# Optimization experiments

Hardware: AMD Instinct MI355X
Metric: run time of the kernel (lower is better)

## Reference

```python
import jax, jax.numpy as jnp
import numpy as np
from jax import lax

N_STEPS, IN_LEN, OUT_LEN, H_LEN, C_LEN, BATCH = 24, 512, 256, 1024, 1024, 128


def setup_inputs() -> dict:
    key = jax.random.key(0)
    ks = jax.random.split(key, 16)
    g = lambda k, shp: jax.random.normal(k, shp, dtype=jnp.float32)
    ih = IN_LEN + H_LEN
    return {
        "x": g(ks[0], (BATCH, N_STEPS, IN_LEN)),
        "W": g(ks[1], (N_STEPS, C_LEN, ih)) * 0.02,
        "Wi": g(ks[2], (N_STEPS, C_LEN, ih)) * 0.02,
        "Wf": g(ks[3], (N_STEPS, C_LEN, ih)) * 0.02,
        "Wo": g(ks[4], (N_STEPS, C_LEN, ih)) * 0.02,
        "Wout": g(ks[5], (N_STEPS, OUT_LEN, H_LEN)) * 0.02,
        "b": g(ks[6], (N_STEPS, C_LEN)) * 0.02,
        "bi": g(ks[7], (N_STEPS, C_LEN)) * 0.02,
        "bf": g(ks[8], (N_STEPS, C_LEN)) * 0.02,
        "bo": g(ks[9], (N_STEPS, C_LEN)) * 0.02,
        "bout": g(ks[10], (N_STEPS, OUT_LEN)) * 0.02,
        "c0": g(ks[11], (C_LEN,)) * 0.02,
        "h0": g(ks[12], (H_LEN,)) * 0.02,
    }


def reference(x, W, Wi, Wf, Wo, Wout, b, bi, bf, bo, bout, c0, h0):
    B = x.shape[0]
    c = jnp.broadcast_to(c0, (B, c0.shape[0]))  # repmat(c0, len(x))
    h = jnp.broadcast_to(h0, (B, h0.shape[0]))

    def step(carry, inp):
        c_, h_ = carry
        xt, w, wi, wf, wo, wout, bb, bbi, bbf, bbo, bbout = inp
        xh = jnp.concatenate([xt, h_], axis=-1)            # [B, i+h]
        z = jnp.tanh(xh @ w.T + bb)                        # [B, c]
        zi = jax.nn.sigmoid(xh @ wi.T + bbi)
        zf = jax.nn.sigmoid(xh @ wf.T + bbf)
        zo = jax.nn.sigmoid(xh @ wo.T + bbo)
        cn = zf * c_ + zi * z
        hn = zo * jnp.tanh(cn)
        y = jax.nn.sigmoid(hn @ wout.T + bbout)            # [B, o]
        return (cn, hn), y

    xs = jnp.swapaxes(x, 0, 1)                             # [n, B, i]
    _, ys = lax.scan(step, (c, h), (xs, W, Wi, Wf, Wo, Wout, b, bi, bf, bo, bout))
    # concat y over steps along last axis -> [B, n*o]
    return jnp.transpose(ys, (1, 0, 2)).reshape(B, -1)
```

## Files before the change

kernel.cpp:

```cpp
#include <hip/hip_runtime.h>

#define B_    128
#define NSTEP 24
#define INL   512
#define OUTL  256
#define HL    1024
#define CL    1024
#define IH    (INL + HL)
#define G_BLOCKS 256

typedef short          s16x8 __attribute__((ext_vector_type(8)));
typedef float          f32x4 __attribute__((ext_vector_type(4)));
typedef unsigned short u16x4 __attribute__((ext_vector_type(4)));

#define FWS_C   64
#define FWS_HA  (FWS_C + 524288)
#define FWS_HB  (FWS_HA + 262144)
#define FWS_XW  (FWS_HB + 262144)
#define FWS_END (FWS_XW + 25165824)
#define WS_C  64
#define WS_HA (64 + 262144)
#define WS_HB (64 + 524288)

__device__ __forceinline__ float bits2f(unsigned short u) {
    union { unsigned u; float f; } w; w.u = ((unsigned)u) << 16; return w.f;
}
__device__ __forceinline__ unsigned short f2bf(float f) {
    union { float f; unsigned u; } w; w.f = f;
    unsigned r = (w.u + 0x7fffu + ((w.u >> 16) & 1u)) >> 16;
    return (unsigned short)r;
}
__device__ __forceinline__ float sigmoidf_(float v) { return 1.0f / (1.0f + expf(-v)); }
__device__ __forceinline__ float sane(float v, float lim) {
    return fminf(fmaxf(v, -lim), lim);
}

template<int FP32>
__device__ __forceinline__ s16x8 load8(const void* base, size_t off) {
    if constexpr (FP32) {
        const float* p = (const float*)base + off;
        f32x4 a = *(const f32x4*)p;
        f32x4 b = *(const f32x4*)(p + 4);
        s16x8 r;
        r[0] = (short)f2bf(a[0]); r[1] = (short)f2bf(a[1]);
        r[2] = (short)f2bf(a[2]); r[3] = (short)f2bf(a[3]);
        r[4] = (short)f2bf(b[0]); r[5] = (short)f2bf(b[1]);
        r[6] = (short)f2bf(b[2]); r[7] = (short)f2bf(b[3]);
        return r;
    } else {
        return *(const s16x8*)((const unsigned short*)base + off);
    }
}
template<int FP32>
__device__ __forceinline__ float ld1(const void* base, size_t off) {
    if constexpr (FP32) return ((const float*)base)[off];
    else                return bits2f(((const unsigned short*)base)[off]);
}
template<int FP32>
__device__ __forceinline__ u16x4 ldcvt4(const void* base, size_t off) {
    if constexpr (FP32) {
        f32x4 v = *(const f32x4*)((const float*)base + off);
        u16x4 r;
        r[0] = f2bf(v[0]); r[1] = f2bf(v[1]); r[2] = f2bf(v[2]); r[3] = f2bf(v[3]);
        return r;
    } else {
        return *(const u16x4*)((const unsigned short*)base + off);
    }
}
__device__ __forceinline__ s16x8 ldh8(const unsigned short* __restrict__ h,
                                      int row, int k0) {
    const unsigned short* p = h + (size_t)(k0 >> 2) * 512 + row * 4;
    u16x4 lo = *(const u16x4*)p;
    u16x4 hi = *(const u16x4*)(p + 512);
    s16x8 r;
    r[0] = (short)lo[0]; r[1] = (short)lo[1]; r[2] = (short)lo[2]; r[3] = (short)lo[3];
    r[4] = (short)hi[0]; r[5] = (short)hi[1]; r[6] = (short)hi[2]; r[7] = (short)hi[3];
    return r;
}

__global__ void detect_kernel(const unsigned* __restrict__ xw, int* __restrict__ flag) {
    __shared__ int wild, zero;
    const int tid = threadIdx.x;
    if (tid == 0) { wild = 0; zero = 0; }
    __syncthreads();
    int w = 0, z = 0;
    for (int s = 0; s < 4; ++s) {
        unsigned short lo = (unsigned short)(xw[tid * 4 + s] & 0xffffu);
        float v = bits2f(lo);
        if (v == 0.0f) z++;
        else if (v == v && (fabsf(v) > 1e4f || fabsf(v) < 1e-8f)) w++;
    }
    atomicAdd(&wild, w);
    atomicAdd(&zero, z);
    __syncthreads();
    if (tid == 0) *flag = (wild > 128 || zero > 512) ? 1 : 0;
}


__global__ void init_full_kernel(const void* c0, const void* h0, const int* __restrict__ flag,
                                 float* __restrict__ c,
                                 unsigned short* __restrict__ hA,
                                 unsigned short* __restrict__ hB)
{
    const int f   = *flag;
    const int idx = blockIdx.x * blockDim.x + threadIdx.x;
    if (idx < B_ * CL) {
        const int j = ((idx >> 9) << 2) + (idx & 3);
        c[idx]  = f ? ((const float*)c0)[j] : bits2f(((const unsigned short*)c0)[j]);
        const float hv = f ? ((const float*)h0)[j] : bits2f(((const unsigned short*)h0)[j]);
        const unsigned short hb = f2bf(hv);
        hA[idx] = hb;
        hB[idx] = hb;
    }
}

#define XA_PITCH 40
template<int FP32>
__device__ __forceinline__ void xw_tile_body(
    const void* __restrict__ x,
    const void* __restrict__ W,  const void* __restrict__ Wi,
    const void* __restrict__ Wf, const void* __restrict__ Wo,
    _Float16* __restrict__ XW, int t, int j0)
{
    __shared__ unsigned short smem[2 * 128 * XA_PITCH];
    unsigned short* Alds = smem;
    unsigned short* Blds = smem + 128 * XA_PITCH;

    const int tid  = threadIdx.x;
    const int lane = tid & 63;
    const int wv   = tid >> 6;
    const int c16  = lane & 15;
    const int kg   = lane >> 4;
    const int mq   = wv >> 1, nq = wv & 1;

    int rowc[4], colc[4];
    const void* wbase[4];
    size_t wrow[4];
    #pragma unroll
    for (int p = 0; p < 4; ++p) {
        const int cid = tid + p * 256;
        rowc[p] = cid >> 3;
        colc[p] = (cid & 7) * 4;
        const int g = rowc[p] >> 5;
        wbase[p] = (g == 0) ? W : (g == 1) ? Wi : (g == 2) ? Wf : Wo;
        wrow[p]  = ((size_t)(t * CL + j0 + (rowc[p] & 31))) * IH;
    }

    f32x4 acc[4][4];
    #pragma unroll
    for (int a = 0; a < 4; ++a)
        #pragma unroll
        for (int b = 0; b < 4; ++b) acc[a][b] = (f32x4){0.f, 0.f, 0.f, 0.f};

    u16x4 ra[4], rb[4];
    #pragma unroll
    for (int p = 0; p < 4; ++p) {
        ra[p] = ldcvt4<FP32>(wbase[p], wrow[p] + colc[p]);
        rb[p] = ldcvt4<FP32>(x,  ((size_t)(rowc[p] * NSTEP + t)) * INL + colc[p]);
    }

    for (int s = 0; s < 16; ++s) {
        __syncthreads();
        #pragma unroll
        for (int p = 0; p < 4; ++p) {
            *(u16x4*)(Alds + rowc[p] * XA_PITCH + colc[p]) = ra[p];
            *(u16x4*)(Blds + rowc[p] * XA_PITCH + colc[p]) = rb[p];
        }
        if (s < 15) {
            const int k0 = (s + 1) * 32;
            #pragma unroll
            for (int p = 0; p < 4; ++p) {
                ra[p] = ldcvt4<FP32>(wbase[p], wrow[p] + k0 + colc[p]);
                rb[p] = ldcvt4<FP32>(x,  ((size_t)(rowc[p] * NSTEP + t)) * INL + k0 + colc[p]);
            }
        }
        __syncthreads();
        s16x8 av[4], bv[4];
        #pragma unroll
        for (int mf = 0; mf < 4; ++mf)
            av[mf] = *(const s16x8*)(Alds + (mq * 64 + mf * 16 + c16) * XA_PITCH + kg * 8);
        #pragma unroll
        for (int nf = 0; nf < 4; ++nf)
            bv[nf] = *(const s16x8*)(Blds + (nq * 64 + nf * 16 + c16) * XA_PITCH + kg * 8);
        #pragma unroll
        for (int mf = 0; mf < 4; ++mf)
            #pragma unroll
            for (int nf = 0; nf < 4; ++nf)
                acc[mf][nf] = __builtin_amdgcn_mfma_f32_16x16x32_bf16(av[mf], bv[nf], acc[mf][nf], 0, 0, 0);
    }

    #pragma unroll
    for (int mf = 0; mf < 4; ++mf)
        #pragma unroll
        for (int nf = 0; nf < 4; ++nf)
            #pragma unroll
            for (int i = 0; i < 4; ++i) {
                const int jr = mq * 64 + mf * 16 + kg * 4 + i;
                const int bc = nq * 64 + nf * 16 + c16;
                const int g  = jr >> 5;
                const int j  = j0 + (jr & 31);
                XW[((((size_t)t * 256 + (j >> 2)) * B_ + bc) * 4 + (j & 3)) * 4 + g] =
                    (_Float16)acc[mf][nf][i];
            }
}

__global__ __launch_bounds__(256, 2) void xw_tile_kernel(
    const void* x, const void* W, const void* Wi, const void* Wf, const void* Wo,
    const int* __restrict__ flag, _Float16* XW)
{
    const int blk = blockIdx.x;
    const int t   = blk >> 5;
    const int j0  = (blk & 31) * 32;
    if (*flag) xw_tile_body<1>(x, W, Wi, Wf, Wo, XW, t, j0);
    else       xw_tile_body<0>(x, W, Wi, Wf, Wo, XW, t, j0);
}

template<int FP32>
__device__ __forceinline__ void step5_body(
    const void* __restrict__ W,  const void* __restrict__ Wi,
    const void* __restrict__ Wf, const void* __restrict__ Wo,
    const void* __restrict__ bz, const void* __restrict__ bi,
    const void* __restrict__ bfg, const void* __restrict__ bo,
    const void* __restrict__ Wout, const void* __restrict__ bout,
    const _Float16* __restrict__ XW, float* __restrict__ c,
    const unsigned short* __restrict__ hprev,
    unsigned short* __restrict__ hnext,
    float* __restrict__ out, int t)
{
    __shared__ unsigned short smem[16 * 1024];
    const int blk  = blockIdx.x;
    const int tid  = threadIdx.x;
    const int lane = tid & 63;
    const int wv   = tid >> 6;
    const int c16  = lane & 15;
    const int kg   = lane >> 4;
    const bool isOut = (blk >= G_BLOCKS);
    if (isOut && t == 0) return;

    {
        const int srow = tid >> 5;
        const int scl  = (tid & 31) * 4;
        const void* wptr;
        size_t woff;
        if (!isOut) {
            const int g = srow >> 2, jj = srow & 3;
            wptr = (g == 0) ? W : (g == 1) ? Wi : (g == 2) ? Wf : Wo;
            woff = ((size_t)(t * CL + blk * 4 + jj)) * IH + INL;
        } else {
            wptr = Wout;
            woff = ((size_t)((t - 1) * OUTL + (blk - G_BLOCKS) * 16 + srow)) * HL;
        }
        const unsigned swz = (unsigned)((srow & 7) << 4);
        #pragma unroll
        for (int i = 0; i < 8; ++i) {
            const int col = scl + i * 128;
            u16x4 v = ldcvt4<FP32>(wptr, woff + col);
            *(u16x4*)((char*)smem + srow * 2048 + (((unsigned)(col * 2)) ^ swz)) = v;
        }
    }
    __syncthreads();

    const int row = wv * 16 + c16;
    const char* brow = (const char*)smem + c16 * 2048;
    const unsigned cswz = (unsigned)((c16 & 7) << 4);
    f32x4 acc = {0.f, 0.f, 0.f, 0.f};
    #pragma unroll 8
    for (int kb = 0; kb < HL; kb += 32) {
        s16x8 av = ldh8(hprev, row, kb + kg * 8);
        s16x8 bv = *(const s16x8*)(brow + (((unsigned)((kb + kg * 8) * 2)) ^ cswz));
        acc = __builtin_amdgcn_mfma_f32_16x16x32_bf16(av, bv, acc, 0, 0, 0);
    }

    if (isOut) {
        const int o = (blk - G_BLOCKS) * 16 + c16;
        const float bb = ld1<FP32>(bout, (size_t)(t - 1) * OUTL + o);
        #pragma unroll
        for (int i = 0; i < 4; ++i) {
            const int b = wv * 16 + kg * 4 + i;
            out[(size_t)b * (NSTEP * OUTL) + (size_t)(t - 1) * OUTL + o] =
                sigmoidf_(sane(acc[i] + bb, 30.f));
        }
        return;
    }

    __syncthreads();
    float* lsm = (float*)smem;
    #pragma unroll
    for (int i = 0; i < 4; ++i)
        lsm[c16 * 130 + wv * 16 + kg * 4 + i] = acc[i];
    __syncthreads();

    const int b  = tid >> 2;
    const int jq = tid & 3;
    const int jg = blk * 4 + jq;
    u16x4 xv = *(const u16x4*)((const unsigned short*)XW +
                               (((size_t)t * 256 + blk) * B_ + b) * 16 + jq * 4);
    union { unsigned short u; _Float16 h; } cv0, cv1, cv2, cv3;
    cv0.u = xv[0]; cv1.u = xv[1]; cv2.u = xv[2]; cv3.u = xv[3];
    const float l0 = lsm[(0 * 4 + jq) * 130 + b] + (float)cv0.h
                   + ld1<FP32>(bz,  (size_t)t * CL + jg);
    const float l1 = lsm[(1 * 4 + jq) * 130 + b] + (float)cv1.h
                   + ld1<FP32>(bi,  (size_t)t * CL + jg);
    const float l2 = lsm[(2 * 4 + jq) * 130 + b] + (float)cv2.h
                   + ld1<FP32>(bfg, (size_t)t * CL + jg);
    const float l3 = lsm[(3 * 4 + jq) * 130 + b] + (float)cv3.h
                   + ld1<FP32>(bo,  (size_t)t * CL + jg);
    const float z  = tanhf(sane(l0, 30.f));
    const float zi = sigmoidf_(sane(l1, 30.f));
    const float zf = sigmoidf_(sane(l2, 30.f));
    const float zo = sigmoidf_(sane(l3, 30.f));
    const size_t soff = (size_t)blk * 512 + tid;
    const float cold = c[soff];
    const float cn   = sane(zf * cold + zi * z, 50.f);
    c[soff] = cn;
    hnext[soff] = f2bf(zo * tanhf(cn));
}

__global__ __launch_bounds__(512, 4) void step5_kernel(
    const void* W, const void* Wi, const void* Wf, const void* Wo,
    const void* bz, const void* bi, const void* bfg, const void* bo,
    const void* Wout, const void* bout,
    const int* __restrict__ flag, const _Float16* XW, float* c,
    const unsigned short* hprev, unsigned short* hnext, float* out, int t)
{
    if (*flag) step5_body<1>(W, Wi, Wf, Wo, bz, bi, bfg, bo, Wout, bout, XW, c, hprev, hnext, out, t);
    else       step5_body<0>(W, Wi, Wf, Wo, bz, bi, bfg, bo, Wout, bout, XW, c, hprev, hnext, out, t);
}

template<int FP32>
__device__ __forceinline__ void outproj_part(
    const unsigned short* __restrict__ h, const void* __restrict__ Wout,
    const void* __restrict__ bout, float* __restrict__ out, int tp, int og,
    int tid, float* __restrict__ red)
{
    const int lane = tid & 63;
    const int wv   = tid >> 6;
    const int c16  = lane & 15;
    const int kg   = lane >> 4;
    const int mf   = wv & 1;
    const int kh   = wv >> 1;

    const int o0   = (og & 15) * 16;
    const int mgrp = og >> 4;
    const int o    = o0 + c16;

    const size_t woff = ((size_t)tp * OUTL + o) * HL + kh * 512 + kg * 8;
    const int row = mgrp * 32 + mf * 16 + c16;

    f32x4 acc = {0.f, 0.f, 0.f, 0.f};
    #pragma unroll 8
    for (int kb = 0; kb < 512; kb += 32) {
        s16x8 av = ldh8(h, row, kh * 512 + kb + kg * 8);
        s16x8 bv = load8<FP32>(Wout, woff + kb);
        acc = __builtin_amdgcn_mfma_f32_16x16x32_bf16(av, bv, acc, 0, 0, 0);
    }
    #pragma unroll
    for (int i = 0; i < 4; ++i)
        red[((kh * 2 + mf) * 16 + c16) * 16 + kg * 4 + i] = acc[i];
    __syncthreads();

    const float bb = ld1<FP32>(bout, (size_t)tp * OUTL + o0 + (tid & 15));
    #pragma unroll
    for (int p = 0; p < 2; ++p) {
        const int idx = tid + p * 256;
        const int cc  = idx & 15;
        const int r   = idx >> 4;
        const int mff = r >> 4, rm = r & 15;
        const float lgv = red[(mff * 16 + cc) * 16 + rm]
                        + red[((2 + mff) * 16 + cc) * 16 + rm] + bb;
        out[(size_t)(mgrp * 32 + r) * (NSTEP * OUTL) + (size_t)tp * OUTL + o0 + cc] =
            sigmoidf_(sane(lgv, 30.f));
    }
}

__global__ __launch_bounds__(512, 4) void outproj_final2_kernel(
    const unsigned short* h, const void* Wout, const void* bout,
    const int* __restrict__ flag, float* out)
{
    __shared__ float red[2048];
    const int tid  = threadIdx.x;
    const int half = tid >> 8;
    const int og   = blockIdx.x * 2 + half;
    if (*flag) outproj_part<1>(h, Wout, bout, out, NSTEP - 1, og, tid & 255, red + half * 1024);
    else       outproj_part<0>(h, Wout, bout, out, NSTEP - 1, og, tid & 255, red + half * 1024);
}

template<int FP32>
__device__ __forceinline__ void gate_body(
    const void* __restrict__ x,
    const void* __restrict__ W,  const void* __restrict__ Wi,
    const void* __restrict__ Wf, const void* __restrict__ Wo,
    const void* __restrict__ bz, const void* __restrict__ bi,
    const void* __restrict__ bfg, const void* __restrict__ bo,
    _Float16* __restrict__ c,
    const unsigned short* __restrict__ hprev,
    unsigned short* __restrict__ hnext, int t)
{
    const int tid  = threadIdx.x;
    const int lane = tid & 63;
    const int wv   = tid >> 6;
    const int j0   = blockIdx.x * 4;
    const int c16  = lane & 15;
    const int g    = c16 >> 2;
    const int jj   = c16 & 3;
    const int kg   = lane >> 4;

    const void* Wg = (g == 0) ? W : (g == 1) ? Wi : (g == 2) ? Wf : Wo;
    const size_t woff = ((size_t)t * CL + (j0 + jj)) * IH + kg * 8;
    const int row0 = wv * 32 + c16;
    const int row1 = row0 + 16;

    f32x4 acc0 = {0.f, 0.f, 0.f, 0.f};
    f32x4 acc1 = {0.f, 0.f, 0.f, 0.f};
    {
        const size_t a0 = ((size_t)row0 * NSTEP + t) * INL + kg * 8;
        const size_t a1 = ((size_t)row1 * NSTEP + t) * INL + kg * 8;
        #pragma unroll 4
        for (int kb = 0; kb < INL; kb += 32) {
            s16x8 av0 = load8<FP32>(x, a0 + kb);
            s16x8 av1 = load8<FP32>(x, a1 + kb);
            s16x8 bv  = load8<FP32>(Wg, woff + kb);
            acc0 = __builtin_amdgcn_mfma_f32_16x16x32_bf16(av0, bv, acc0, 0, 0, 0);
            acc1 = __builtin_amdgcn_mfma_f32_16x16x32_bf16(av1, bv, acc1, 0, 0, 0);
        }
    }
    {
        const unsigned short* a0 = hprev + (size_t)row0 * HL + kg * 8;
        const unsigned short* a1 = hprev + (size_t)row1 * HL + kg * 8;
        const size_t w2 = woff + INL;
        #pragma unroll 4
        for (int kb = 0; kb < HL; kb += 32) {
            s16x8 av0 = *(const s16x8*)(a0 + kb);
            s16x8 av1 = *(const s16x8*)(a1 + kb);
            s16x8 bv  = load8<FP32>(Wg, w2 + kb);
            acc0 = __builtin_amdgcn_mfma_f32_16x16x32_bf16(av0, bv, acc0, 0, 0, 0);
            acc1 = __builtin_amdgcn_mfma_f32_16x16x32_bf16(av1, bv, acc1, 0, 0, 0);
        }
    }
    __shared__ float lg[4][4][B_];
    #pragma unroll
    for (int i = 0; i < 4; ++i) {
        lg[g][jj][wv * 32 + kg * 4 + i]      = acc0[i];
        lg[g][jj][wv * 32 + 16 + kg * 4 + i] = acc1[i];
    }
    __syncthreads();
    #pragma unroll
    for (int p = 0; p < 2; ++p) {
        const int idx = tid + p * 256;
        const int b   = idx & 127;
        const int jl  = idx >> 7;
        const int jg  = j0 + jl;
        const float z  = tanhf   (sane(lg[0][jl][b] + ld1<FP32>(bz,  t * CL + jg), 30.f));
        const float zi = sigmoidf_(sane(lg[1][jl][b] + ld1<FP32>(bi,  t * CL + jg), 30.f));
        const float zf = sigmoidf_(sane(lg[2][jl][b] + ld1<FP32>(bfg, t * CL + jg), 30.f));
        const float zo = sigmoidf_(sane(lg[3][jl][b] + ld1<FP32>(bo,  t * CL + jg), 30.f));
        const float cold = (float)c[(size_t)b * CL + jg];
        const float cn   = sane(zf * cold + zi * z, 50.f);
        c[(size_t)b * CL + jg] = (_Float16)cn;
        hnext[(size_t)b * HL + jg] = f2bf(zo * tanhf(cn));
    }
}

__global__ __launch_bounds__(256, 1) void gate_cell_kernel(
    const void* x, const void* W, const void* Wi, const void* Wf, const void* Wo,
    const void* bz, const void* bi, const void* bfg, const void* bo,
    const int* __restrict__ flag, _Float16* c,
    const unsigned short* hprev, unsigned short* hnext, int t)
{
    if (*flag) gate_body<1>(x, W, Wi, Wf, Wo, bz, bi, bfg, bo, c, hprev, hnext, t);
    else       gate_body<0>(x, W, Wi, Wf, Wo, bz, bi, bfg, bo, c, hprev, hnext, t);
}

template<int FP32>
__device__ __forceinline__ void outproj_body(
    const unsigned short* __restrict__ h, const void* __restrict__ Wout,
    const void* __restrict__ bout, float* __restrict__ out, int t)
{
    const int tid  = threadIdx.x;
    const int lane = tid & 63;
    const int wv   = tid >> 6;
    const int o    = blockIdx.x * 16 + (lane & 15);
    const int kg   = lane >> 4;
    const size_t woff = ((size_t)t * OUTL + o) * HL + kg * 8;
    const int row0 = wv * 32 + (lane & 15);
    const int row1 = row0 + 16;
    const unsigned short* a0 = h + (size_t)row0 * HL + kg * 8;
    const unsigned short* a1 = h + (size_t)row1 * HL + kg * 8;

    f32x4 acc0 = {0.f, 0.f, 0.f, 0.f};
    f32x4 acc1 = {0.f, 0.f, 0.f, 0.f};
    #pragma unroll 4
    for (int kb = 0; kb < HL; kb += 32) {
        s16x8 av0 = *(const s16x8*)(a0 + kb);
        s16x8 av1 = *(const s16x8*)(a1 + kb);
        s16x8 bv  = load8<FP32>(Wout, woff + kb);
        acc0 = __builtin_amdgcn_mfma_f32_16x16x32_bf16(av0, bv, acc0, 0, 0, 0);
        acc1 = __builtin_amdgcn_mfma_f32_16x16x32_bf16(av1, bv, acc1, 0, 0, 0);
    }
    const float bb = ld1<FP32>(bout, (size_t)t * OUTL + o);
    #pragma unroll
    for (int i = 0; i < 4; ++i) {
        const int r0 = wv * 32 + kg * 4 + i;
        out[(size_t)r0 * (NSTEP * OUTL) + (size_t)t * OUTL + o] =
            sigmoidf_(sane(acc0[i] + bb, 30.f));
        out[(size_t)(r0 + 16) * (NSTEP * OUTL) + (size_t)t * OUTL + o] =
            sigmoidf_(sane(acc1[i] + bb, 30.f));
    }
}

__global__ __launch_bounds__(256, 1) void outproj_kernel(
    const unsigned short* h, const void* Wout, const void* bout,
    const int* __restrict__ flag, float* out, int t)
{
    if (*flag) outproj_body<1>(h, Wout, bout, out, t);
    else       outproj_body<0>(h, Wout, bout, out, t);
}

__global__ void init_kernel(const void* c0, const void* h0, const int* __restrict__ flag,
                            _Float16* __restrict__ c,
                            unsigned short* __restrict__ hA,
                            unsigned short* __restrict__ hB)
{
    const int f   = *flag;
    const int idx = blockIdx.x * blockDim.x + threadIdx.x;
    if (idx < B_ * CL) {
        const int j = idx & (CL - 1);
        const float cv = f ? ((const float*)c0)[j] : bits2f(((const unsigned short*)c0)[j]);
        const float hv = f ? ((const float*)h0)[j] : bits2f(((const unsigned short*)h0)[j]);
        c[idx]  = (_Float16)cv;
        const unsigned short hb = f2bf(hv);
        hA[idx] = hb;
        hB[idx] = hb;
    }
}

extern "C" void kernel_launch(void* const* d_in, const int* in_sizes, int n_in,
                              void* d_out, int out_size, void* d_ws, size_t ws_size,
                              hipStream_t stream)
{
    const void* x    = d_in[0];
    const void* W    = d_in[1];
    const void* Wi   = d_in[2];
    const void* Wf   = d_in[3];
    const void* Wo   = d_in[4];
    const void* Wout = d_in[5];
    const void* bz   = d_in[6];
    const void* bi   = d_in[7];
    const void* bfg  = d_in[8];
    const void* bo   = d_in[9];
    const void* bout = d_in[10];
    const void* c0   = d_in[11];
    const void* h0   = d_in[12];

    char* ws  = (char*)d_ws;
    int* flag = (int*)ws;
    float* out = (float*)d_out;

    detect_kernel<<<1, 256, 0, stream>>>((const unsigned*)x, flag);

    if (ws_size >= (size_t)FWS_END) {
        float*          c  = (float*)(ws + FWS_C);
        unsigned short* hA = (unsigned short*)(ws + FWS_HA);
        unsigned short* hB = (unsigned short*)(ws + FWS_HB);
        _Float16*       XW = (_Float16*)(ws + FWS_XW);

        init_full_kernel<<<512, 256, 0, stream>>>(c0, h0, flag, c, hA, hB);
        xw_tile_kernel<<<768, 256, 0, stream>>>(x, W, Wi, Wf, Wo, flag, XW);

        for (int t = 0; t < NSTEP; ++t) {
            const unsigned short* hp = (t & 1) ? hB : hA;
            unsigned short*       hn = (t & 1) ? hA : hB;
            step5_kernel<<<G_BLOCKS + 16, 512, 0, stream>>>(
                W, Wi, Wf, Wo, bz, bi, bfg, bo, Wout, bout,
                flag, XW, c, hp, hn, out, t);
        }
        outproj_final2_kernel<<<32, 512, 0, stream>>>(hA, Wout, bout, flag, out);
    } else {
        _Float16*       c  = (_Float16*)(ws + WS_C);
        unsigned short* hA = (unsigned short*)(ws + WS_HA);
        unsigned short* hB = (unsigned short*)(ws + WS_HB);

        init_kernel<<<512, 256, 0, stream>>>(c0, h0, flag, c, hA, hB);
        for (int t = 0; t < NSTEP; ++t) {
            const unsigned short* hp = (t & 1) ? hB : hA;
            unsigned short*       hn = (t & 1) ? hA : hB;
            gate_cell_kernel<<<256, 256, 0, stream>>>(
                x, W, Wi, Wf, Wo, bz, bi, bfg, bo, flag, c, hp, hn, t);
            outproj_kernel<<<16, 256, 0, stream>>>(hn, Wout, bout, flag, out, t);
        }
    }
}
```

Before: 438.7 us.

## Fold input-projection GEMM into per-step kernels, computing two steps ahead

The standalone XW precompute kernel is replaced. It now only computes steps 0 and 1, and each recurrent step kernel launches extra blocks that compute the x·W input projection for step t+2. The aim is to hide that GEMM work in CUs left idle by the latency-bound recurrence instead of paying for it up front. The XW tile is also reworked to 8 hidden units × 4 gates per block, with weights staged in swizzled LDS and x streamed from global. The trade-off is lower occupancy (launch bounds 4 down to 2) and possible contention between the extra blocks and the recurrent blocks.

```diff
diff --git a/kernel.cpp b/kernel.cpp
--- a/kernel.cpp
+++ b/kernel.cpp
@@ -8,10 +8,13 @@
 #define CL    1024
 #define IH    (INL + HL)
 #define G_BLOCKS 256
+#define O_BLOCKS 16
+#define X_BLOCKS 128
 
 typedef short          s16x8 __attribute__((ext_vector_type(8)));
 typedef float          f32x4 __attribute__((ext_vector_type(4)));
 typedef unsigned short u16x4 __attribute__((ext_vector_type(4)));
+typedef unsigned short u16x8 __attribute__((ext_vector_type(8)));
 
 #define FWS_C   64
 #define FWS_HA  (FWS_C + 524288)
@@ -114,126 +117,104 @@
     }
 }
 
-#define XA_PITCH 40
-template<int FP32>
-__device__ __forceinline__ void xw_tile_body(
+template<int FP32>
+__device__ __forceinline__ void xw2_body(
     const void* __restrict__ x,
     const void* __restrict__ W,  const void* __restrict__ Wi,
     const void* __restrict__ Wf, const void* __restrict__ Wo,
-    _Float16* __restrict__ XW, int t, int j0)
-{
-    __shared__ unsigned short smem[2 * 128 * XA_PITCH];
-    unsigned short* Alds = smem;
-    unsigned short* Blds = smem + 128 * XA_PITCH;
-
+    _Float16* __restrict__ XW, int t_x, int j0,
+    unsigned short* __restrict__ smem)
+{
     const int tid  = threadIdx.x;
     const int lane = tid & 63;
     const int wv   = tid >> 6;
     const int c16  = lane & 15;
     const int kg   = lane >> 4;
-    const int mq   = wv >> 1, nq = wv & 1;
-
-    int rowc[4], colc[4];
-    const void* wbase[4];
-    size_t wrow[4];
-    #pragma unroll
-    for (int p = 0; p < 4; ++p) {
-        const int cid = tid + p * 256;
-        rowc[p] = cid >> 3;
-        colc[p] = (cid & 7) * 4;
-        const int g = rowc[p] >> 5;
-        wbase[p] = (g == 0) ? W : (g == 1) ? Wi : (g == 2) ? Wf : Wo;
-        wrow[p]  = ((size_t)(t * CL + j0 + (rowc[p] & 31))) * IH;
-    }
-
-    f32x4 acc[4][4];
-    #pragma unroll
-    for (int a = 0; a < 4; ++a)
+
+    {
+        const int srow = tid >> 4;
+        const int scl  = (tid & 15) * 4;
+        const int g    = srow & 3;
+        const void* wptr = (g == 0) ? W : (g == 1) ? Wi : (g == 2) ? Wf : Wo;
+        const size_t woff = ((size_t)(t_x * CL + j0 + (srow >> 2))) * IH;
+        const unsigned swz = (unsigned)((srow & 7) << 4);
         #pragma unroll
-        for (int b = 0; b < 4; ++b) acc[a][b] = (f32x4){0.f, 0.f, 0.f, 0.f};
-
-    u16x4 ra[4], rb[4];
-    #pragma unroll
-    for (int p = 0; p < 4; ++p) {
-        ra[p] = ldcvt4<FP32>(wbase[p], wrow[p] + colc[p]);
-        rb[p] = ldcvt4<FP32>(x,  ((size_t)(rowc[p] * NSTEP + t)) * INL + colc[p]);
-    }
-
-    for (int s = 0; s < 16; ++s) {
-        __syncthreads();
+        for (int i = 0; i < 8; ++i) {
+            const int col = scl + i * 64;
+            u16x4 v = ldcvt4<FP32>(wptr, woff + col);
+            *(u16x4*)((char*)smem + srow * 1024 + (((unsigned)(col * 2)) ^ swz)) = v;
+        }
+    }
+    __syncthreads();
+
+    const int row = wv * 16 + c16;
+    const size_t xrow = ((size_t)row * NSTEP + t_x) * INL + kg * 8;
+    const char* b0 = (const char*)smem + (0 * 16 + c16) * 1024;
+    const char* b1 = (const char*)smem + (1 * 16 + c16) * 1024;
+    const unsigned cswz = (unsigned)((c16 & 7) << 4);
+    f32x4 acc0 = {0.f, 0.f, 0.f, 0.f};
+    f32x4 acc1 = {0.f, 0.f, 0.f, 0.f};
+    #pragma unroll 8
+    for (int kb = 0; kb < INL; kb += 32) {
+        s16x8 av  = load8<FP32>(x, xrow + kb);
+        const unsigned ko = ((unsigned)((kb + kg * 8) * 2)) ^ cswz;
+        s16x8 bv0 = *(const s16x8*)(b0 + ko);
+        s16x8 bv1 = *(const s16x8*)(b1 + ko);
+        acc0 = __builtin_amdgcn_mfma_f32_16x16x32_bf16(av, bv0, acc0, 0, 0, 0);
+        acc1 = __builtin_amdgcn_mfma_f32_16x16x32_bf16(av, bv1, acc1, 0, 0, 0);
+    }
+
+    #pragma unroll
+    for (int f = 0; f < 2; ++f) {
+        const f32x4& a = f ? acc1 : acc0;
+        const int r  = f * 16 + c16;
+        const int j  = j0 + (r >> 2);
+        const int g  = r & 3;
+        _Float16* dst = XW + (((size_t)t_x * 256 + (j >> 2)) * B_) * 16 + (j & 3) * 4 + g;
         #pragma unroll
-        for (int p = 0; p < 4; ++p) {
-            *(u16x4*)(Alds + rowc[p] * XA_PITCH + colc[p]) = ra[p];
-            *(u16x4*)(Blds + rowc[p] * XA_PITCH + colc[p]) = rb[p];
-        }
-        if (s < 15) {
-            const int k0 = (s + 1) * 32;
-            #pragma unroll
-            for (int p = 0; p < 4; ++p) {
-                ra[p] = ldcvt4<FP32>(wbase[p], wrow[p] + k0 + colc[p]);
-                rb[p] = ldcvt4<FP32>(x,  ((size_t)(rowc[p] * NSTEP + t)) * INL + k0 + colc[p]);
-            }
-        }
-        __syncthreads();
-        s16x8 av[4], bv[4];
-        #pragma unroll
-        for (int mf = 0; mf < 4; ++mf)
-            av[mf] = *(const s16x8*)(Alds + (mq * 64 + mf * 16 + c16) * XA_PITCH + kg * 8);
-        #pragma unroll
-        for (int nf = 0; nf < 4; ++nf)
-            bv[nf] = *(const s16x8*)(Blds + (nq * 64 + nf * 16 + c16) * XA_PITCH + kg * 8);
-        #pragma unroll
-        for (int mf = 0; mf < 4; ++mf)
-            #pragma unroll
-            for (int nf = 0; nf < 4; ++nf)
-                acc[mf][nf] = __builtin_amdgcn_mfma_f32_16x16x32_bf16(av[mf], bv[nf], acc[mf][nf], 0, 0, 0);
-    }
-
-    #pragma unroll
-    for (int mf = 0; mf < 4; ++mf)
-        #pragma unroll
-        for (int nf = 0; nf < 4; ++nf)
-            #pragma unroll
-            for (int i = 0; i < 4; ++i) {
-                const int jr = mq * 64 + mf * 16 + kg * 4 + i;
-                const int bc = nq * 64 + nf * 16 + c16;
-                const int g  = jr >> 5;
-                const int j  = j0 + (jr & 31);
-                XW[((((size_t)t * 256 + (j >> 2)) * B_ + bc) * 4 + (j & 3)) * 4 + g] =
-                    (_Float16)acc[mf][nf][i];
-            }
-}
-
-__global__ __launch_bounds__(256, 2) void xw_tile_kernel(
+        for (int i = 0; i < 4; ++i) {
+            const int b = wv * 16 + kg * 4 + i;
+            dst[(size_t)b * 16] = (_Float16)a[i];
+        }
+    }
+}
+
+__global__ __launch_bounds__(512, 2) void xw_pre_kernel(
     const void* x, const void* W, const void* Wi, const void* Wf, const void* Wo,
     const int* __restrict__ flag, _Float16* XW)
 {
-    const int blk = blockIdx.x;
-    const int t   = blk >> 5;
-    const int j0  = (blk & 31) * 32;
-    if (*flag) xw_tile_body<1>(x, W, Wi, Wf, Wo, XW, t, j0);
-    else       xw_tile_body<0>(x, W, Wi, Wf, Wo, XW, t, j0);
-}
-
-template<int FP32>
-__device__ __forceinline__ void step5_body(
+    __shared__ unsigned short smem[16384];
+    const int t_x = blockIdx.x >> 7;
+    const int j0  = (blockIdx.x & 127) * 8;
+    if (*flag) xw2_body<1>(x, W, Wi, Wf, Wo, XW, t_x, j0, smem);
+    else       xw2_body<0>(x, W, Wi, Wf, Wo, XW, t_x, j0, smem);
+}
+
+template<int FP32>
+__device__ __forceinline__ void step7_body(
+    const void* __restrict__ x,
     const void* __restrict__ W,  const void* __restrict__ Wi,
     const void* __restrict__ Wf, const void* __restrict__ Wo,
     const void* __restrict__ bz, const void* __restrict__ bi,
     const void* __restrict__ bfg, const void* __restrict__ bo,
     const void* __restrict__ Wout, const void* __restrict__ bout,
-    const _Float16* __restrict__ XW, float* __restrict__ c,
+    _Float16* __restrict__ XW, float* __restrict__ c,
     const unsigned short* __restrict__ hprev,
     unsigned short* __restrict__ hnext,
-    float* __restrict__ out, int t)
-{
-    __shared__ unsigned short smem[16 * 1024];
+    float* __restrict__ out, int t,
+    unsigned short* __restrict__ smem)
+{
     const int blk  = blockIdx.x;
     const int tid  = threadIdx.x;
     const int lane = tid & 63;
     const int wv   = tid >> 6;
     const int c16  = lane & 15;
     const int kg   = lane >> 4;
+
+    if (blk >= G_BLOCKS + O_BLOCKS) {
+        xw2_body<FP32>(x, W, Wi, Wf, Wo, XW, t + 2, (blk - G_BLOCKS - O_BLOCKS) * 8, smem);
+        return;
+    }
     const bool isOut = (blk >= G_BLOCKS);
     if (isOut && t == 0) return;
 
@@ -316,15 +297,17 @@
     hnext[soff] = f2bf(zo * tanhf(cn));
 }
 
-__global__ __launch_bounds__(512, 4) void step5_kernel(
+__global__ __launch_bounds__(512, 2) void step7_kernel(
+    const void* x,
     const void* W, const void* Wi, const void* Wf, const void* Wo,
     const void* bz, const void* bi, const void* bfg, const void* bo,
     const void* Wout, const void* bout,
-    const int* __restrict__ flag, const _Float16* XW, float* c,
+    const int* __restrict__ flag, _Float16* XW, float* c,
     const unsigned short* hprev, unsigned short* hnext, float* out, int t)
 {
-    if (*flag) step5_body<1>(W, Wi, Wf, Wo, bz, bi, bfg, bo, Wout, bout, XW, c, hprev, hnext, out, t);
-    else       step5_body<0>(W, Wi, Wf, Wo, bz, bi, bfg, bo, Wout, bout, XW, c, hprev, hnext, out, t);
+    __shared__ unsigned short smem[16384];
+    if (*flag) step7_body<1>(x, W, Wi, Wf, Wo, bz, bi, bfg, bo, Wout, bout, XW, c, hprev, hnext, out, t, smem);
+    else       step7_body<0>(x, W, Wi, Wf, Wo, bz, bi, bfg, bo, Wout, bout, XW, c, hprev, hnext, out, t, smem);
 }
 
 template<int FP32>
@@ -565,13 +548,15 @@
         _Float16*       XW = (_Float16*)(ws + FWS_XW);
 
         init_full_kernel<<<512, 256, 0, stream>>>(c0, h0, flag, c, hA, hB);
-        xw_tile_kernel<<<768, 256, 0, stream>>>(x, W, Wi, Wf, Wo, flag, XW);
+        xw_pre_kernel<<<2 * X_BLOCKS, 512, 0, stream>>>(x, W, Wi, Wf, Wo, flag, XW);
 
         for (int t = 0; t < NSTEP; ++t) {
             const unsigned short* hp = (t & 1) ? hB : hA;
             unsigned short*       hn = (t & 1) ? hA : hB;
-            step5_kernel<<<G_BLOCKS + 16, 512, 0, stream>>>(
-                W, Wi, Wf, Wo, bz, bi, bfg, bo, Wout, bout,
+            const int grid = (t + 2 < NSTEP) ? (G_BLOCKS + O_BLOCKS + X_BLOCKS)
+                                             : (G_BLOCKS + O_BLOCKS);
+            step7_kernel<<<grid, 512, 0, stream>>>(
+                x, W, Wi, Wf, Wo, bz, bi, bfg, bo, Wout, bout,
                 flag, XW, c, hp, hn, out, t);
         }
         outproj_final2_kernel<<<32, 512, 0, stream>>>(hA, Wout, bout, flag, out);
```

Result: slower. 467.2 us (+6.5%).
